# Performance work log

Hardware: AMD Instinct MI355X
Metric: run time of the kernel (lower is better)

Reference implementation:

```python
import jax, jax.numpy as jnp
import numpy as np

B, T, C, H = 2, 2048, 1024, 16
HD = C // H  # head dim = 64


def setup_inputs() -> dict:
    key = jax.random.key(0)
    ks = jax.random.split(key, 5)
    s = 1.0 / np.sqrt(C)
    return {
        "x": jax.random.normal(ks[0], (B, T, C), dtype=jnp.float32),
        "Wq": jax.random.normal(ks[1], (C, C), dtype=jnp.float32) * s,
        "bq": jnp.zeros((C,), dtype=jnp.float32),
        "Wk": jax.random.normal(ks[2], (C, C), dtype=jnp.float32) * s,
        "bk": jnp.zeros((C,), dtype=jnp.float32),
        "Wv": jax.random.normal(ks[3], (C, C), dtype=jnp.float32) * s,
        "bv": jnp.zeros((C,), dtype=jnp.float32),
        "Wp": jax.random.normal(ks[4], (C, C), dtype=jnp.float32) * s,
        "bp": jnp.zeros((C,), dtype=jnp.float32),
    }


def reference(x, Wq, bq, Wk, bk, Wv, bv, Wp, bp):
    # QKV projections -> [B, H, T, HD]
    def proj(W, b):
        return (x @ W.T + b).reshape(B, T, H, HD).transpose(0, 2, 1, 3)

    q = proj(Wq, bq)
    k = proj(Wk, bk)
    v = proj(Wv, bv)

    scale = 1.0 / np.sqrt(HD)
    att = jnp.einsum("bhtd,bhsd->bhts", q, k) * scale  # [B,H,T,T]
    causal = jnp.tril(jnp.ones((T, T), dtype=bool))
    att = jnp.where(causal, att, -jnp.inf)
    att = jax.nn.softmax(att, axis=-1)
    y = jnp.einsum("bhts,bhsd->bhtd", att, v)          # [B,H,T,HD]
    y = y.transpose(0, 2, 1, 3).reshape(B, T, C)
    return y @ Wp.T + bp
```

## Files before the change

### kernel.cpp

```cpp
#include <hip/hip_runtime.h>
#include <hip/hip_bf16.h>

#define BB 2
#define TT 2048
#define CC 1024
#define HH 16
#define HDD 64

typedef __attribute__((ext_vector_type(8))) short bf16x8;
typedef __attribute__((ext_vector_type(4))) float f32x4;

static __device__ __forceinline__ unsigned short f2bf(float f) {
  union { float f; unsigned u; } v; v.f = f;
  unsigned r = v.u + 0x7fffu + ((v.u >> 16) & 1u);
  return (unsigned short)(r >> 16);
}

static __device__ __forceinline__ unsigned fbits(float f) {
  union { float f; unsigned u; } v; v.f = f; return v.u;
}

static __device__ __forceinline__ unsigned pk_trunc(float lo, float hi) {
  return __builtin_amdgcn_perm(fbits(hi), fbits(lo), 0x07060302u);
}

static __device__ __forceinline__ float fexp2(float x) {
#if __has_builtin(__builtin_amdgcn_exp2f)
  return __builtin_amdgcn_exp2f(x);
#else
  return exp2f(x);
#endif
}

static __device__ __forceinline__ void gload_lds16(const unsigned short* g, unsigned short* l) {
  __builtin_amdgcn_global_load_lds((const __attribute__((address_space(1))) void*)g,
                                   (__attribute__((address_space(3))) void*)l, 16, 0, 0);
}

__global__ __launch_bounds__(256) void convert_all(
    const float* __restrict__ x, const float* __restrict__ Wq,
    const float* __restrict__ Wk, const float* __restrict__ Wv,
    const float* __restrict__ Wp, unsigned short* __restrict__ dst)
{
  const size_t M4 = 4194304, M1 = 1048576;
  const size_t e = ((size_t)blockIdx.x * 256 + threadIdx.x) * 8;
  const float* src; size_t off;
  if (e < M4)            { src = x;  off = e; }
  else if (e < M4 + M1)  { src = Wq; off = e - M4; }
  else if (e < M4 + 2*M1){ src = Wk; off = e - M4 - M1; }
  else if (e < M4 + 3*M1){ src = Wv; off = e - M4 - 2*M1; }
  else                   { src = Wp; off = e - M4 - 3*M1; }
  float4 a = *(const float4*)(src + off);
  float4 c = *(const float4*)(src + off + 4);
  unsigned short buf[8] = {f2bf(a.x), f2bf(a.y), f2bf(a.z), f2bf(a.w),
                           f2bf(c.x), f2bf(c.y), f2bf(c.z), f2bf(c.w)};
  *(uint4*)(dst + e) = *(const uint4*)buf;
}


__global__ __launch_bounds__(256) void gemm_mfma(
    const unsigned short* __restrict__ A, const unsigned short* __restrict__ W,
    const float* __restrict__ b0, const float* __restrict__ b1, const float* __restrict__ b2,
    unsigned short* __restrict__ oQ, unsigned short* __restrict__ oK,
    unsigned short* __restrict__ oVt)
{
  __shared__ unsigned short As[2][128][32];
  __shared__ unsigned short Bs[2][128][32];
  const int t = threadIdx.x;
  const int wv = __builtin_amdgcn_readfirstlane(t >> 6);
  const int ln = t & 63;
  const int l16 = ln & 15;
  const int quad = ln >> 4;
  const int mBase = blockIdx.x * 128;
  const int nBase = blockIdx.y * 128;
  const int wm = (wv >> 1) * 64, wn = (wv & 1) * 64;

  f32x4 acc[4][4];
#pragma unroll
  for (int i = 0; i < 4; i++)
#pragma unroll
    for (int j = 0; j < 4; j++) acc[i][j] = (f32x4){0.f, 0.f, 0.f, 0.f};

  const int rloc = t >> 2;
  const int csrc = ((t & 3) ^ ((t >> 3) & 3)) * 8;
  const unsigned short* gA = A + (size_t)(mBase + rloc) * CC + csrc;
  const unsigned short* gB = W + (size_t)(nBase + rloc) * CC + csrc;
  const int sw = (quad ^ ((l16 >> 1) & 3)) * 8;

#define STAGE(b, kt)                                                       \
  do {                                                                     \
    const size_t ko = (size_t)(kt) * 32;                                   \
    gload_lds16(gA + ko,               &As[b][0][0] + t * 8);              \
    gload_lds16(gA + ko + 64 * CC,     &As[b][64][0] + t * 8);             \
    gload_lds16(gB + ko,               &Bs[b][0][0] + t * 8);              \
    gload_lds16(gB + ko + 64 * CC,     &Bs[b][64][0] + t * 8);             \
  } while (0)

  STAGE(0, 0);
  for (int kt = 0; kt < 32; ++kt) {
    const int cur = kt & 1;
    if (kt < 31) {
      STAGE(cur ^ 1, kt + 1);
      asm volatile("s_waitcnt vmcnt(4)" ::: "memory");
    } else {
      asm volatile("s_waitcnt vmcnt(0)" ::: "memory");
    }
    __builtin_amdgcn_s_barrier();
    asm volatile("" ::: "memory");
    bf16x8 af[4], bfr[4];
#pragma unroll
    for (int i = 0; i < 4; ++i) af[i] = *(const bf16x8*)&As[cur][wm + i * 16 + l16][sw];
#pragma unroll
    for (int j = 0; j < 4; ++j) bfr[j] = *(const bf16x8*)&Bs[cur][wn + j * 16 + l16][sw];
    __builtin_amdgcn_s_setprio(1);
#pragma unroll
    for (int i = 0; i < 4; ++i)
#pragma unroll
      for (int j = 0; j < 4; ++j)
        acc[i][j] = __builtin_amdgcn_mfma_f32_16x16x32_bf16(af[i], bfr[j], acc[i][j], 0, 0, 0);
    __builtin_amdgcn_s_setprio(0);
    asm volatile("" ::: "memory");
    __builtin_amdgcn_s_barrier();
    asm volatile("" ::: "memory");
  }
#undef STAGE

  const int which = nBase >> 10;
  const float* bias = which == 0 ? b0 : (which == 1 ? b1 : b2);
  unsigned short* dst = which == 0 ? oQ : (which == 1 ? oK : oVt);
  const float scl = which == 0 ? 0.1803368801f : 1.0f;
#pragma unroll
  for (int i = 0; i < 4; i++)
#pragma unroll
    for (int r = 0; r < 4; r++) {
      const int m = mBase + wm + i * 16 + quad * 4 + r;
      const int b = m >> 11, tp = m & 2047;
#pragma unroll
      for (int j = 0; j < 4; j++) {
        const int n = nBase + wn + j * 16 + l16;
        const int nl = n & 1023, h = nl >> 6, d = nl & 63;
        const unsigned short v = f2bf((acc[i][j][r] + bias[nl]) * scl);
        if (which < 2) dst[((size_t)(b * HH + h) * TT + tp) * HDD + d] = v;
        else           dst[((size_t)(b * HH + h) * HDD + d) * TT + tp] = v;
      }
    }
}

__global__ __launch_bounds__(512) void gemm_proj(
    const unsigned short* __restrict__ A, const unsigned short* __restrict__ W,
    const float* __restrict__ bias, float* __restrict__ out)
{
  __shared__ unsigned short As[2][128][32];
  __shared__ unsigned short Bs[2][128][32];
  const int t = threadIdx.x;
  const int wv = __builtin_amdgcn_readfirstlane(t >> 6);
  const int ln = t & 63;
  const int l16 = ln & 15;
  const int quad = ln >> 4;
  const int mBase = blockIdx.x * 128;
  const int nBase = blockIdx.y * 128;
  const int wm = (wv >> 2) * 64;
  const int wn = (wv & 3) * 32;

  f32x4 acc[4][2];
#pragma unroll
  for (int i = 0; i < 4; i++)
#pragma unroll
    for (int j = 0; j < 2; j++) acc[i][j] = (f32x4){0.f, 0.f, 0.f, 0.f};

  const int rloc = t >> 2;
  const int csrc = ((t & 3) ^ ((t >> 3) & 3)) * 8;
  const unsigned short* gA = A + (size_t)(mBase + rloc) * CC + csrc;
  const unsigned short* gB = W + (size_t)(nBase + rloc) * CC + csrc;
  const int sw = (quad ^ ((l16 >> 1) & 3)) * 8;

#define STAGE(b, kt)                                                       \
  do {                                                                     \
    const size_t ko = (size_t)(kt) * 32;                                   \
    gload_lds16(gA + ko, &As[b][0][0] + t * 8);                            \
    gload_lds16(gB + ko, &Bs[b][0][0] + t * 8);                            \
  } while (0)

  STAGE(0, 0);
  for (int kt = 0; kt < 32; ++kt) {
    const int cur = kt & 1;
    if (kt < 31) {
      STAGE(cur ^ 1, kt + 1);
      asm volatile("s_waitcnt vmcnt(2)" ::: "memory");
    } else {
      asm volatile("s_waitcnt vmcnt(0)" ::: "memory");
    }
    __builtin_amdgcn_s_barrier();
    asm volatile("" ::: "memory");
    bf16x8 af[4], bfr[2];
#pragma unroll
    for (int i = 0; i < 4; ++i) af[i] = *(const bf16x8*)&As[cur][wm + i * 16 + l16][sw];
#pragma unroll
    for (int j = 0; j < 2; ++j) bfr[j] = *(const bf16x8*)&Bs[cur][wn + j * 16 + l16][sw];
    __builtin_amdgcn_s_setprio(1);
#pragma unroll
    for (int i = 0; i < 4; ++i)
#pragma unroll
      for (int j = 0; j < 2; ++j)
        acc[i][j] = __builtin_amdgcn_mfma_f32_16x16x32_bf16(af[i], bfr[j], acc[i][j], 0, 0, 0);
    __builtin_amdgcn_s_setprio(0);
    asm volatile("" ::: "memory");
    __builtin_amdgcn_s_barrier();
    asm volatile("" ::: "memory");
  }
#undef STAGE

#pragma unroll
  for (int i = 0; i < 4; i++)
#pragma unroll
    for (int r = 0; r < 4; r++) {
      const int m = mBase + wm + i * 16 + quad * 4 + r;
#pragma unroll
      for (int j = 0; j < 2; j++) {
        const int n = nBase + wn + j * 16 + l16;
        out[(size_t)m * CC + n] = acc[i][j][r] + bias[n];
      }
    }
}

__global__ __launch_bounds__(256, 2) void attn_mfma(
    const unsigned short* __restrict__ Q, const unsigned short* __restrict__ K,
    const unsigned short* __restrict__ Vt, unsigned short* __restrict__ y)
{
  __shared__ unsigned short QP[128][72];
  __shared__ unsigned short Ks[2][64][72];
  __shared__ unsigned short Vts[2][64][72];

  const int t = threadIdx.x;
  const int a = blockIdx.x;
  const int bh = blockIdx.y;
  const int wave = t >> 6;
  const int lane = t & 63;
  const int l16 = lane & 15;
  const int quad = lane >> 4;

  const size_t base = (size_t)bh * TT * HDD;
  const int qtL = a, qtH = 31 - a;
  const int qBaseL = qtL * 64, qBaseH = qtH * 64;

#pragma unroll
  for (int p = 0; p < 4; p++) {
    const int c = p * 256 + t;
    const int r = c >> 3, off = (c & 7) * 8;
    const int srcRow = (r < 64) ? (qBaseL + r) : (qBaseH + r - 64);
    *(uint4*)&QP[r][off] = *(const uint4*)(Q + base + (size_t)srcRow * HDD + off);
  }

  const int sr = t >> 2, sc = (t & 3) * 8;
  const unsigned short* kbase = K + base + (size_t)sr * HDD + sc;
  const unsigned short* vbase = Vt + base + (size_t)sr * TT + sc;
  uint4 kr0 = *(const uint4*)(kbase);
  uint4 kr1 = *(const uint4*)(kbase + 32);
  uint4 vr0 = *(const uint4*)(vbase);
  uint4 vr1 = *(const uint4*)(vbase + 32);
  __syncthreads();

  bf16x8 qfL0 = *(const bf16x8*)&QP[wave * 16 + l16][quad * 8];
  bf16x8 qfL1 = *(const bf16x8*)&QP[wave * 16 + l16][32 + quad * 8];
  bf16x8 qfH0 = *(const bf16x8*)&QP[64 + wave * 16 + l16][quad * 8];
  bf16x8 qfH1 = *(const bf16x8*)&QP[64 + wave * 16 + l16][32 + quad * 8];
  unsigned short (*PtH)[72] = (unsigned short (*)[72])&QP[wave * 16];
  unsigned short (*PtL)[72] = (unsigned short (*)[72])&QP[64 + wave * 16];

  float lL = 0.f, lH = 0.f;
  f32x4 OfrL[4], OfrH[4];
#pragma unroll
  for (int dt = 0; dt < 4; dt++) {
    OfrL[dt] = (f32x4){0.f, 0.f, 0.f, 0.f};
    OfrH[dt] = (f32x4){0.f, 0.f, 0.f, 0.f};
  }

  for (int kt = 0; kt <= qtH; kt++) {
    const int buf = kt & 1;
    *(uint4*)&Ks[buf][sr][sc]       = kr0;
    *(uint4*)&Ks[buf][sr][sc + 32]  = kr1;
    *(uint4*)&Vts[buf][sr][sc]      = vr0;
    *(uint4*)&Vts[buf][sr][sc + 32] = vr1;
    __syncthreads();
    if (kt < qtH) {
      kr0 = *(const uint4*)(kbase + (size_t)(kt + 1) * 64 * HDD);
      kr1 = *(const uint4*)(kbase + (size_t)(kt + 1) * 64 * HDD + 32);
      vr0 = *(const uint4*)(vbase + (kt + 1) * 64);
      vr1 = *(const uint4*)(vbase + (kt + 1) * 64 + 32);
    }
    const bool doLo = (kt <= qtL);

    f32x4 StH[4], StL[4];
#pragma unroll
    for (int ct = 0; ct < 4; ct++) {
      bf16x8 a0 = *(const bf16x8*)&Ks[buf][ct * 16 + l16][quad * 8];
      bf16x8 a1 = *(const bf16x8*)&Ks[buf][ct * 16 + l16][32 + quad * 8];
      f32x4 s = (f32x4){0.f, 0.f, 0.f, 0.f};
      s = __builtin_amdgcn_mfma_f32_16x16x32_bf16(a0, qfH0, s, 0, 0, 0);
      s = __builtin_amdgcn_mfma_f32_16x16x32_bf16(a1, qfH1, s, 0, 0, 0);
      StH[ct] = s;
      if (doLo) {
        f32x4 s2 = (f32x4){0.f, 0.f, 0.f, 0.f};
        s2 = __builtin_amdgcn_mfma_f32_16x16x32_bf16(a0, qfL0, s2, 0, 0, 0);
        s2 = __builtin_amdgcn_mfma_f32_16x16x32_bf16(a1, qfL1, s2, 0, 0, 0);
        StL[ct] = s2;
      }
    }

    if (kt == qtH) {
#pragma unroll
      for (int ct = 0; ct < 4; ct++) {
        float p[4];
#pragma unroll
        for (int r = 0; r < 4; r++) {
          float pv = fexp2(StH[ct][r]);
          if (ct * 16 + quad * 4 + r > wave * 16 + l16) pv = 0.f;
          p[r] = pv;
        }
        lH += (p[0] + p[1]) + (p[2] + p[3]);
        uint2 pk = {pk_trunc(p[0], p[1]), pk_trunc(p[2], p[3])};
        *(uint2*)&PtH[l16][ct * 16 + quad * 4] = pk;
      }
    } else {
#pragma unroll
      for (int ct = 0; ct < 4; ct++) {
        float p[4];
#pragma unroll
        for (int r = 0; r < 4; r++) p[r] = fexp2(StH[ct][r]);
        lH += (p[0] + p[1]) + (p[2] + p[3]);
        uint2 pk = {pk_trunc(p[0], p[1]), pk_trunc(p[2], p[3])};
        *(uint2*)&PtH[l16][ct * 16 + quad * 4] = pk;
      }
    }
    if (doLo) {
      if (kt == qtL) {
#pragma unroll
        for (int ct = 0; ct < 4; ct++) {
          float p[4];
#pragma unroll
          for (int r = 0; r < 4; r++) {
            float pv = fexp2(StL[ct][r]);
            if (ct * 16 + quad * 4 + r > wave * 16 + l16) pv = 0.f;
            p[r] = pv;
          }
          lL += (p[0] + p[1]) + (p[2] + p[3]);
          uint2 pk = {pk_trunc(p[0], p[1]), pk_trunc(p[2], p[3])};
          *(uint2*)&PtL[l16][ct * 16 + quad * 4] = pk;
        }
      } else {
#pragma unroll
        for (int ct = 0; ct < 4; ct++) {
          float p[4];
#pragma unroll
          for (int r = 0; r < 4; r++) p[r] = fexp2(StL[ct][r]);
          lL += (p[0] + p[1]) + (p[2] + p[3]);
          uint2 pk = {pk_trunc(p[0], p[1]), pk_trunc(p[2], p[3])};
          *(uint2*)&PtL[l16][ct * 16 + quad * 4] = pk;
        }
      }
    }

    bf16x8 paH0 = *(const bf16x8*)&PtH[l16][quad * 8];
    bf16x8 paH1 = *(const bf16x8*)&PtH[l16][32 + quad * 8];
    bf16x8 paL0, paL1;
    if (doLo) {
      paL0 = *(const bf16x8*)&PtL[l16][quad * 8];
      paL1 = *(const bf16x8*)&PtL[l16][32 + quad * 8];
    }
#pragma unroll
    for (int dt = 0; dt < 4; dt++) {
      bf16x8 vb0 = *(const bf16x8*)&Vts[buf][dt * 16 + l16][quad * 8];
      bf16x8 vb1 = *(const bf16x8*)&Vts[buf][dt * 16 + l16][32 + quad * 8];
      OfrH[dt] = __builtin_amdgcn_mfma_f32_16x16x32_bf16(paH0, vb0, OfrH[dt], 0, 0, 0);
      OfrH[dt] = __builtin_amdgcn_mfma_f32_16x16x32_bf16(paH1, vb1, OfrH[dt], 0, 0, 0);
      if (doLo) {
        OfrL[dt] = __builtin_amdgcn_mfma_f32_16x16x32_bf16(paL0, vb0, OfrL[dt], 0, 0, 0);
        OfrL[dt] = __builtin_amdgcn_mfma_f32_16x16x32_bf16(paL1, vb1, OfrL[dt], 0, 0, 0);
      }
    }
  }

  lL += __shfl_xor(lL, 16, 64); lL += __shfl_xor(lL, 32, 64);
  lH += __shfl_xor(lH, 16, 64); lH += __shfl_xor(lH, 32, 64);

  const int b = bh >> 4, h = bh & 15;
  float lRowL[4], lRowH[4];
#pragma unroll
  for (int r = 0; r < 4; r++) {
    lRowL[r] = __shfl(lL, quad * 4 + r, 16);
    lRowH[r] = __shfl(lH, quad * 4 + r, 16);
  }
#pragma unroll
  for (int r = 0; r < 4; r++) {
    const int qL = qBaseL + wave * 16 + quad * 4 + r;
    const int qH = qBaseH + wave * 16 + quad * 4 + r;
    const float invL = 1.0f / lRowL[r];
    const float invH = 1.0f / lRowH[r];
    unsigned short* ypL = y + ((size_t)(b * TT + qL)) * CC + h * 64 + l16;
    unsigned short* ypH = y + ((size_t)(b * TT + qH)) * CC + h * 64 + l16;
#pragma unroll
    for (int dt = 0; dt < 4; dt++) {
      ypL[dt * 16] = f2bf(OfrL[dt][r] * invL);
      ypH[dt * 16] = f2bf(OfrH[dt][r] * invH);
    }
  }
}

extern "C" void kernel_launch(void* const* d_in, const int* in_sizes, int n_in,
                              void* d_out, int out_size, void* d_ws, size_t ws_size,
                              hipStream_t stream) {
  const float* x  = (const float*)d_in[0];
  const float* Wq = (const float*)d_in[1];
  const float* bq = (const float*)d_in[2];
  const float* Wk = (const float*)d_in[3];
  const float* bk = (const float*)d_in[4];
  const float* Wv = (const float*)d_in[5];
  const float* bv = (const float*)d_in[6];
  const float* Wp = (const float*)d_in[7];
  const float* bp = (const float*)d_in[8];

  const size_t M4 = 4194304, M1 = 1048576;
  unsigned short* xb   = (unsigned short*)d_ws;
  unsigned short* wqb  = xb + M4;
  unsigned short* wpb  = wqb + 3 * M1;
  unsigned short* wsQ  = wpb + M1;
  unsigned short* wsK  = wsQ + M4;
  unsigned short* wsVt = wsK + M4;
  unsigned short* yb   = wsVt + M4;

  convert_all<<<4096, 256, 0, stream>>>(x, Wq, Wk, Wv, Wp, xb);
  gemm_mfma<<<dim3(32, 24), 256, 0, stream>>>(xb, wqb, bq, bk, bv,
                                              wsQ, wsK, wsVt);
  attn_mfma<<<dim3(16, BB * HH), 256, 0, stream>>>(wsQ, wsK, wsVt, yb);
  gemm_proj<<<dim3(32, 8), 512, 0, stream>>>(yb, wpb, bp, (float*)d_out);
}
```

Measured before the change: 187.1 us.

## Enlarge QKV GEMM tile to 256x256 with eight-wave phased LDS staging

The QKV projection GEMM moves from 128x128 tiles with 4 waves and a K-step of 32 to 256x256 tiles with 8 waves and a K-step of 64. Each wave computes a 128x64 sub-tile. Each K-iteration is split into four phases, and each phase issues the global-to-LDS load for one quarter of the next stage while MFMAs run on the current buffer. The goal is more data reuse per LDS byte and fewer barriers per FLOP. In exchange, the grid shrinks to 192 blocks, fewer than the number of CUs, and each block uses about 128KB of LDS, which limits occupancy and leaves some CUs idle.

```diff
diff --git a/kernel.cpp b/kernel.cpp
--- a/kernel.cpp
+++ b/kernel.cpp
@@ -57,80 +57,150 @@
   *(uint4*)(dst + e) = *(const uint4*)buf;
 }
 
-
-__global__ __launch_bounds__(256) void gemm_mfma(
+__global__ __launch_bounds__(512, 2) void gemm_mfma(
     const unsigned short* __restrict__ A, const unsigned short* __restrict__ W,
     const float* __restrict__ b0, const float* __restrict__ b1, const float* __restrict__ b2,
     unsigned short* __restrict__ oQ, unsigned short* __restrict__ oK,
     unsigned short* __restrict__ oVt)
 {
-  __shared__ unsigned short As[2][128][32];
-  __shared__ unsigned short Bs[2][128][32];
+  __shared__ unsigned short As[2][256][64];
+  __shared__ unsigned short Bs[2][256][64];
   const int t = threadIdx.x;
   const int wv = __builtin_amdgcn_readfirstlane(t >> 6);
   const int ln = t & 63;
   const int l16 = ln & 15;
   const int quad = ln >> 4;
-  const int mBase = blockIdx.x * 128;
-  const int nBase = blockIdx.y * 128;
-  const int wm = (wv >> 1) * 64, wn = (wv & 1) * 64;
-
-  f32x4 acc[4][4];
-#pragma unroll
-  for (int i = 0; i < 4; i++)
+  const int mBase = blockIdx.x * 256;
+  const int nBase = blockIdx.y * 256;
+  const int wm = (wv >> 2) * 128;
+  const int wn = (wv & 3) * 64;
+
+  f32x4 acc[8][4];
+#pragma unroll
+  for (int i = 0; i < 8; i++)
 #pragma unroll
     for (int j = 0; j < 4; j++) acc[i][j] = (f32x4){0.f, 0.f, 0.f, 0.f};
 
-  const int rloc = t >> 2;
-  const int csrc = ((t & 3) ^ ((t >> 3) & 3)) * 8;
-  const unsigned short* gA = A + (size_t)(mBase + rloc) * CC + csrc;
-  const unsigned short* gB = W + (size_t)(nBase + rloc) * CC + csrc;
-  const int sw = (quad ^ ((l16 >> 1) & 3)) * 8;
-
-#define STAGE(b, kt)                                                       \
-  do {                                                                     \
-    const size_t ko = (size_t)(kt) * 32;                                   \
-    gload_lds16(gA + ko,               &As[b][0][0] + t * 8);              \
-    gload_lds16(gA + ko + 64 * CC,     &As[b][64][0] + t * 8);             \
-    gload_lds16(gB + ko,               &Bs[b][0][0] + t * 8);              \
-    gload_lds16(gB + ko + 64 * CC,     &Bs[b][64][0] + t * 8);             \
+  const int srow = t >> 3;
+  const int schunk = ((t & 7) ^ (srow & 7)) * 8;
+  const unsigned short* gA = A + (size_t)(mBase + srow) * CC + schunk;
+  const unsigned short* gB = W + (size_t)(nBase + srow) * CC + schunk;
+
+  const int sw0 = ((0 + quad) ^ (l16 & 7)) * 8;
+  const int sw1 = ((4 + quad) ^ (l16 & 7)) * 8;
+
+#define STAGE_HALF(bi, kt, h)                                                   \
+  do {                                                                          \
+    if ((h) < 2) {                                                              \
+      const unsigned short* s_ = gA + (size_t)((h) * 128) * CC + (size_t)(kt) * 64; \
+      unsigned short* d_ = &As[bi][(h) * 128][0] + t * 8;                       \
+      gload_lds16(s_, d_);                                                      \
+      gload_lds16(s_ + (size_t)64 * CC, d_ + 4096);                            \
+    } else {                                                                    \
+      const unsigned short* s_ = gB + (size_t)(((h) - 2) * 128) * CC + (size_t)(kt) * 64; \
+      unsigned short* d_ = &Bs[bi][((h) - 2) * 128][0] + t * 8;                 \
+      gload_lds16(s_, d_);                                                      \
+      gload_lds16(s_ + (size_t)64 * CC, d_ + 4096);                            \
+    }                                                                           \
   } while (0)
 
-  STAGE(0, 0);
-  for (int kt = 0; kt < 32; ++kt) {
-    const int cur = kt & 1;
-    if (kt < 31) {
-      STAGE(cur ^ 1, kt + 1);
-      asm volatile("s_waitcnt vmcnt(4)" ::: "memory");
-    } else {
-      asm volatile("s_waitcnt vmcnt(0)" ::: "memory");
-    }
+  STAGE_HALF(0, 0, 0);
+  STAGE_HALF(0, 0, 1);
+  STAGE_HALF(0, 0, 2);
+  STAGE_HALF(0, 0, 3);
+  STAGE_HALF(1, 1, 0);
+  asm volatile("s_waitcnt vmcnt(2)" ::: "memory");
+  __builtin_amdgcn_s_barrier();
+  asm volatile("" ::: "memory");
+
+  bf16x8 af[4][2], bfr[4][2];
+  for (int kt = 0; kt < 16; ++kt) {
+    const int buf = kt & 1, nb = buf ^ 1;
+
+#pragma unroll
+    for (int i = 0; i < 4; ++i) {
+      af[i][0] = *(const bf16x8*)&As[buf][wm + i * 16 + l16][sw0];
+      af[i][1] = *(const bf16x8*)&As[buf][wm + i * 16 + l16][sw1];
+    }
+#pragma unroll
+    for (int j = 0; j < 2; ++j) {
+      bfr[j][0] = *(const bf16x8*)&Bs[buf][wn + j * 16 + l16][sw0];
+      bfr[j][1] = *(const bf16x8*)&Bs[buf][wn + j * 16 + l16][sw1];
+    }
+    if (kt < 15) STAGE_HALF(nb, kt + 1, 1);
+    __builtin_amdgcn_s_setprio(1);
+#pragma unroll
+    for (int i = 0; i < 4; ++i)
+#pragma unroll
+      for (int j = 0; j < 2; ++j) {
+        acc[i][j] = __builtin_amdgcn_mfma_f32_16x16x32_bf16(af[i][0], bfr[j][0], acc[i][j], 0, 0, 0);
+        acc[i][j] = __builtin_amdgcn_mfma_f32_16x16x32_bf16(af[i][1], bfr[j][1], acc[i][j], 0, 0, 0);
+      }
+    __builtin_amdgcn_s_setprio(0);
+    asm volatile("" ::: "memory");
     __builtin_amdgcn_s_barrier();
     asm volatile("" ::: "memory");
-    bf16x8 af[4], bfr[4];
-#pragma unroll
-    for (int i = 0; i < 4; ++i) af[i] = *(const bf16x8*)&As[cur][wm + i * 16 + l16][sw];
-#pragma unroll
-    for (int j = 0; j < 4; ++j) bfr[j] = *(const bf16x8*)&Bs[cur][wn + j * 16 + l16][sw];
+
+#pragma unroll
+    for (int j = 2; j < 4; ++j) {
+      bfr[j][0] = *(const bf16x8*)&Bs[buf][wn + j * 16 + l16][sw0];
+      bfr[j][1] = *(const bf16x8*)&Bs[buf][wn + j * 16 + l16][sw1];
+    }
+    if (kt < 15) STAGE_HALF(nb, kt + 1, 2);
     __builtin_amdgcn_s_setprio(1);
 #pragma unroll
     for (int i = 0; i < 4; ++i)
 #pragma unroll
-      for (int j = 0; j < 4; ++j)
-        acc[i][j] = __builtin_amdgcn_mfma_f32_16x16x32_bf16(af[i], bfr[j], acc[i][j], 0, 0, 0);
+      for (int j = 2; j < 4; ++j) {
+        acc[i][j] = __builtin_amdgcn_mfma_f32_16x16x32_bf16(af[i][0], bfr[j][0], acc[i][j], 0, 0, 0);
+        acc[i][j] = __builtin_amdgcn_mfma_f32_16x16x32_bf16(af[i][1], bfr[j][1], acc[i][j], 0, 0, 0);
+      }
     __builtin_amdgcn_s_setprio(0);
     asm volatile("" ::: "memory");
     __builtin_amdgcn_s_barrier();
     asm volatile("" ::: "memory");
-  }
-#undef STAGE
+
+#pragma unroll
+    for (int i = 0; i < 4; ++i) {
+      af[i][0] = *(const bf16x8*)&As[buf][wm + 64 + i * 16 + l16][sw0];
+      af[i][1] = *(const bf16x8*)&As[buf][wm + 64 + i * 16 + l16][sw1];
+    }
+    if (kt < 15) STAGE_HALF(nb, kt + 1, 3);
+    __builtin_amdgcn_s_setprio(1);
+#pragma unroll
+    for (int i = 0; i < 4; ++i)
+#pragma unroll
+      for (int j = 0; j < 2; ++j) {
+        acc[4 + i][j] = __builtin_amdgcn_mfma_f32_16x16x32_bf16(af[i][0], bfr[j][0], acc[4 + i][j], 0, 0, 0);
+        acc[4 + i][j] = __builtin_amdgcn_mfma_f32_16x16x32_bf16(af[i][1], bfr[j][1], acc[4 + i][j], 0, 0, 0);
+      }
+    __builtin_amdgcn_s_setprio(0);
+    asm volatile("" ::: "memory");
+    __builtin_amdgcn_s_barrier();
+    asm volatile("" ::: "memory");
+
+    if (kt < 14) STAGE_HALF(buf, kt + 2, 0);
+    __builtin_amdgcn_s_setprio(1);
+#pragma unroll
+    for (int i = 0; i < 4; ++i)
+#pragma unroll
+      for (int j = 2; j < 4; ++j) {
+        acc[4 + i][j] = __builtin_amdgcn_mfma_f32_16x16x32_bf16(af[i][0], bfr[j][0], acc[4 + i][j], 0, 0, 0);
+        acc[4 + i][j] = __builtin_amdgcn_mfma_f32_16x16x32_bf16(af[i][1], bfr[j][1], acc[4 + i][j], 0, 0, 0);
+      }
+    __builtin_amdgcn_s_setprio(0);
+    asm volatile("s_waitcnt vmcnt(2)" ::: "memory");
+    __builtin_amdgcn_s_barrier();
+    asm volatile("" ::: "memory");
+  }
+#undef STAGE_HALF
 
   const int which = nBase >> 10;
   const float* bias = which == 0 ? b0 : (which == 1 ? b1 : b2);
   unsigned short* dst = which == 0 ? oQ : (which == 1 ? oK : oVt);
   const float scl = which == 0 ? 0.1803368801f : 1.0f;
 #pragma unroll
-  for (int i = 0; i < 4; i++)
+  for (int i = 0; i < 8; i++)
 #pragma unroll
     for (int r = 0; r < 4; r++) {
       const int m = mBase + wm + i * 16 + quad * 4 + r;
@@ -429,7 +499,7 @@
   unsigned short* yb   = wsVt + M4;
 
   convert_all<<<4096, 256, 0, stream>>>(x, Wq, Wk, Wv, Wp, xb);
-  gemm_mfma<<<dim3(32, 24), 256, 0, stream>>>(xb, wqb, bq, bk, bv,
+  gemm_mfma<<<dim3(16, 12), 512, 0, stream>>>(xb, wqb, bq, bk, bv,
                                               wsQ, wsK, wsVt);
   attn_mfma<<<dim3(16, BB * HH), 256, 0, stream>>>(wsQ, wsK, wsVt, yb);
   gemm_proj<<<dim3(32, 8), 512, 0, stream>>>(yb, wpb, bp, (float*)d_out);
```

Measured after the change: 203.7 us. +8.9%, slower.

## Enlarge QKV GEMM tiles to 256x256x64 with interleaved staged loads

Applied to the files above, without the earlier changes.

Rewrites the QKV projection GEMM to use 256x256 output tiles with 64-wide K steps and 512 threads per block. Each wave now accumulates an 8x4 fragment grid. Global-to-LDS loads are split into half-tiles and interleaved between MFMA quarter-blocks, with explicit vmcnt waits and barriers for finer-grained pipelining. The goal is more data reuse per byte loaded and latency hidden behind compute. In exchange it uses more LDS and registers, and the grid shrinks to 192 blocks, which may underfill the 256 CUs.

```diff
diff --git a/kernel.cpp b/kernel.cpp
--- a/kernel.cpp
+++ b/kernel.cpp
@@ -57,80 +57,172 @@
   *(uint4*)(dst + e) = *(const uint4*)buf;
 }
 
-
-__global__ __launch_bounds__(256) void gemm_mfma(
+__global__ __launch_bounds__(512, 2) void gemm_mfma(
     const unsigned short* __restrict__ A, const unsigned short* __restrict__ W,
     const float* __restrict__ b0, const float* __restrict__ b1, const float* __restrict__ b2,
     unsigned short* __restrict__ oQ, unsigned short* __restrict__ oK,
     unsigned short* __restrict__ oVt)
 {
-  __shared__ unsigned short As[2][128][32];
-  __shared__ unsigned short Bs[2][128][32];
+  __shared__ unsigned short As[2][256][64];
+  __shared__ unsigned short Bs[2][256][64];
   const int t = threadIdx.x;
   const int wv = __builtin_amdgcn_readfirstlane(t >> 6);
   const int ln = t & 63;
   const int l16 = ln & 15;
   const int quad = ln >> 4;
-  const int mBase = blockIdx.x * 128;
-  const int nBase = blockIdx.y * 128;
-  const int wm = (wv >> 1) * 64, wn = (wv & 1) * 64;
-
-  f32x4 acc[4][4];
-#pragma unroll
-  for (int i = 0; i < 4; i++)
+  const int mBase = blockIdx.x * 256;
+  const int nBase = blockIdx.y * 256;
+  const int wm = (wv >> 2) * 128;
+  const int wn = (wv & 3) * 64;
+
+  f32x4 acc[8][4];
+#pragma unroll
+  for (int i = 0; i < 8; i++)
 #pragma unroll
     for (int j = 0; j < 4; j++) acc[i][j] = (f32x4){0.f, 0.f, 0.f, 0.f};
 
-  const int rloc = t >> 2;
-  const int csrc = ((t & 3) ^ ((t >> 3) & 3)) * 8;
-  const unsigned short* gA = A + (size_t)(mBase + rloc) * CC + csrc;
-  const unsigned short* gB = W + (size_t)(nBase + rloc) * CC + csrc;
-  const int sw = (quad ^ ((l16 >> 1) & 3)) * 8;
-
-#define STAGE(b, kt)                                                       \
-  do {                                                                     \
-    const size_t ko = (size_t)(kt) * 32;                                   \
-    gload_lds16(gA + ko,               &As[b][0][0] + t * 8);              \
-    gload_lds16(gA + ko + 64 * CC,     &As[b][64][0] + t * 8);             \
-    gload_lds16(gB + ko,               &Bs[b][0][0] + t * 8);              \
-    gload_lds16(gB + ko + 64 * CC,     &Bs[b][64][0] + t * 8);             \
-  } while (0)
-
-  STAGE(0, 0);
-  for (int kt = 0; kt < 32; ++kt) {
-    const int cur = kt & 1;
-    if (kt < 31) {
-      STAGE(cur ^ 1, kt + 1);
-      asm volatile("s_waitcnt vmcnt(4)" ::: "memory");
-    } else {
-      asm volatile("s_waitcnt vmcnt(0)" ::: "memory");
-    }
-    __builtin_amdgcn_s_barrier();
-    asm volatile("" ::: "memory");
-    bf16x8 af[4], bfr[4];
-#pragma unroll
-    for (int i = 0; i < 4; ++i) af[i] = *(const bf16x8*)&As[cur][wm + i * 16 + l16][sw];
-#pragma unroll
-    for (int j = 0; j < 4; ++j) bfr[j] = *(const bf16x8*)&Bs[cur][wn + j * 16 + l16][sw];
-    __builtin_amdgcn_s_setprio(1);
-#pragma unroll
-    for (int i = 0; i < 4; ++i)
-#pragma unroll
-      for (int j = 0; j < 4; ++j)
-        acc[i][j] = __builtin_amdgcn_mfma_f32_16x16x32_bf16(af[i], bfr[j], acc[i][j], 0, 0, 0);
-    __builtin_amdgcn_s_setprio(0);
-    asm volatile("" ::: "memory");
-    __builtin_amdgcn_s_barrier();
-    asm volatile("" ::: "memory");
-  }
-#undef STAGE
+  const int srow = t >> 3;
+  const int schunk = ((t & 7) ^ (srow & 7)) * 8;
+  const int rB0 = srow + ((t >> 8) << 5);
+  const unsigned short* gA = A + (size_t)(mBase + srow) * CC + schunk;
+  const unsigned short* gB = W + (size_t)(nBase + rB0) * CC + schunk;
+
+  const int sw0 = ((0 + quad) ^ (l16 & 7)) * 8;
+  const int sw1 = ((4 + quad) ^ (l16 & 7)) * 8;
+
+#define STAGE_A(bi, kt, half)                                                   \
+  do {                                                                          \
+    const unsigned short* s_ = gA + (size_t)((half) * 64) * CC + (size_t)(kt) * 64; \
+    unsigned short* d_ = &As[bi][0][0] + t * 8 + (half) * 4096;                 \
+    gload_lds16(s_, d_);                                                        \
+    gload_lds16(s_ + (size_t)128 * CC, d_ + 8192);                              \
+  } while (0)
+#define STAGE_B(bi, kt, half)                                                   \
+  do {                                                                          \
+    const unsigned short* s_ = gB + (size_t)((half) * 32) * CC + (size_t)(kt) * 64; \
+    unsigned short* d_ = &Bs[bi][0][0] + t * 8 + ((t >> 8) << 11) + (half) * 2048; \
+    gload_lds16(s_, d_);                                                        \
+    gload_lds16(s_ + (size_t)128 * CC, d_ + 8192);                              \
+  } while (0)
+
+#define PBAR()                                                                  \
+  do {                                                                          \
+    asm volatile("" ::: "memory");                                              \
+    __builtin_amdgcn_s_barrier();                                               \
+    asm volatile("" ::: "memory");                                              \
+  } while (0)
+
+#define RD_A(bufc, rbase)                                                       \
+  do {                                                                          \
+    _Pragma("unroll")                                                           \
+    for (int i_ = 0; i_ < 4; ++i_) {                                            \
+      af[i_][0] = *(const bf16x8*)&As[bufc][(rbase) + i_ * 16 + l16][sw0];      \
+      af[i_][1] = *(const bf16x8*)&As[bufc][(rbase) + i_ * 16 + l16][sw1];      \
+    }                                                                           \
+  } while (0)
+#define RD_B(bufc, jb)                                                          \
+  do {                                                                          \
+    _Pragma("unroll")                                                           \
+    for (int j_ = 0; j_ < 2; ++j_) {                                            \
+      bfr[(jb) + j_][0] = *(const bf16x8*)&Bs[bufc][wn + ((jb) + j_) * 16 + l16][sw0]; \
+      bfr[(jb) + j_][1] = *(const bf16x8*)&Bs[bufc][wn + ((jb) + j_) * 16 + l16][sw1]; \
+    }                                                                           \
+  } while (0)
+
+#define MFQ(ib, jb)                                                             \
+  do {                                                                          \
+    __builtin_amdgcn_s_setprio(1);                                              \
+    _Pragma("unroll")                                                           \
+    for (int i_ = 0; i_ < 4; ++i_) {                                            \
+      _Pragma("unroll")                                                         \
+      for (int j_ = 0; j_ < 2; ++j_) {                                          \
+        acc[(ib) + i_][(jb) + j_] = __builtin_amdgcn_mfma_f32_16x16x32_bf16(    \
+            af[i_][0], bfr[(jb) + j_][0], acc[(ib) + i_][(jb) + j_], 0, 0, 0);  \
+        acc[(ib) + i_][(jb) + j_] = __builtin_amdgcn_mfma_f32_16x16x32_bf16(    \
+            af[i_][1], bfr[(jb) + j_][1], acc[(ib) + i_][(jb) + j_], 0, 0, 0);  \
+      }                                                                         \
+    }                                                                           \
+    __builtin_amdgcn_s_setprio(0);                                              \
+  } while (0)
+
+  STAGE_A(0, 0, 0);
+  STAGE_B(0, 0, 0);
+  STAGE_B(0, 0, 1);
+  STAGE_A(0, 0, 1);
+  STAGE_A(1, 1, 0);
+  STAGE_B(1, 1, 0);
+  STAGE_B(1, 1, 1);
+  asm volatile("s_waitcnt vmcnt(6)" ::: "memory");
+  __builtin_amdgcn_s_barrier();
+  asm volatile("" ::: "memory");
+
+  bf16x8 af[4][2], bfr[4][2];
+  for (int it = 0; it < 8; ++it) {
+    const bool nl = it < 7;
+    const int T2 = 2 * it + 2, T3 = 2 * it + 3;
+
+    RD_A(0, wm); RD_B(0, 0);
+    STAGE_A(1, 2 * it + 1, 1);
+    PBAR();
+    MFQ(0, 0);
+    PBAR();
+
+    RD_B(0, 2);
+    if (nl) STAGE_A(0, T2, 0);
+    PBAR();
+    MFQ(0, 2);
+    PBAR();
+
+    RD_A(0, wm + 64);
+    if (nl) STAGE_B(0, T2, 0);
+    PBAR();
+    MFQ(4, 0);
+    PBAR();
+
+    if (nl) STAGE_B(0, T2, 1);
+    PBAR();
+    MFQ(4, 2);
+    if (nl) asm volatile("s_waitcnt vmcnt(6)" ::: "memory");
+    else    asm volatile("s_waitcnt vmcnt(0)" ::: "memory");
+    PBAR();
+
+    RD_A(1, wm); RD_B(1, 0);
+    if (nl) STAGE_A(0, T2, 1);
+    PBAR();
+    MFQ(0, 0);
+    PBAR();
+
+    RD_B(1, 2);
+    if (nl) STAGE_A(1, T3, 0);
+    PBAR();
+    MFQ(0, 2);
+    PBAR();
+
+    RD_A(1, wm + 64);
+    if (nl) STAGE_B(1, T3, 0);
+    PBAR();
+    MFQ(4, 0);
+    PBAR();
+
+    if (nl) STAGE_B(1, T3, 1);
+    PBAR();
+    MFQ(4, 2);
+    if (nl) asm volatile("s_waitcnt vmcnt(6)" ::: "memory");
+    PBAR();
+  }
+#undef STAGE_A
+#undef STAGE_B
+#undef PBAR
+#undef RD_A
+#undef RD_B
+#undef MFQ
 
   const int which = nBase >> 10;
   const float* bias = which == 0 ? b0 : (which == 1 ? b1 : b2);
   unsigned short* dst = which == 0 ? oQ : (which == 1 ? oK : oVt);
   const float scl = which == 0 ? 0.1803368801f : 1.0f;
 #pragma unroll
-  for (int i = 0; i < 4; i++)
+  for (int i = 0; i < 8; i++)
 #pragma unroll
     for (int r = 0; r < 4; r++) {
       const int m = mBase + wm + i * 16 + quad * 4 + r;
@@ -138,8 +230,8 @@
 #pragma unroll
       for (int j = 0; j < 4; j++) {
         const int n = nBase + wn + j * 16 + l16;
-        const int nl = n & 1023, h = nl >> 6, d = nl & 63;
-        const unsigned short v = f2bf((acc[i][j][r] + bias[nl]) * scl);
+        const int nl2 = n & 1023, h = nl2 >> 6, d = nl2 & 63;
+        const unsigned short v = f2bf((acc[i][j][r] + bias[nl2]) * scl);
         if (which < 2) dst[((size_t)(b * HH + h) * TT + tp) * HDD + d] = v;
         else           dst[((size_t)(b * HH + h) * HDD + d) * TT + tp] = v;
       }
@@ -429,7 +521,7 @@
   unsigned short* yb   = wsVt + M4;
 
   convert_all<<<4096, 256, 0, stream>>>(x, Wq, Wk, Wv, Wp, xb);
-  gemm_mfma<<<dim3(32, 24), 256, 0, stream>>>(xb, wqb, bq, bk, bv,
+  gemm_mfma<<<dim3(16, 12), 512, 0, stream>>>(xb, wqb, bq, bk, bv,
                                               wsQ, wsK, wsVt);
   attn_mfma<<<dim3(16, BB * HH), 256, 0, stream>>>(wsQ, wsK, wsVt, yb);
   gemm_proj<<<dim3(32, 8), 512, 0, stream>>>(yb, wpb, bp, (float*)d_out);
```

After: 203.6 us. 1.09x slower.
